# Performance work log

Hardware: AMD Instinct MI355X
Metric: run time of the kernel (lower is better)

## Reference

```python
import jax, jax.numpy as jnp
import numpy as np

NUDGE = 1e-7

def _norm(x):
    # global mean + L2-norm over axes (1,2), per sample (faithful to source)
    size = x.shape[1] * x.shape[2]
    mean = jnp.sum(x, axis=(1, 2), keepdims=True) / size
    xc = x - mean
    l2 = jnp.sqrt(jnp.sum(xc * xc, axis=(1, 2), keepdims=True))
    return xc / (l2 + NUDGE)


def setup_inputs() -> dict:
    key = jax.random.key(0)
    ks = jax.random.split(key, 9)
    B, D, S, F = 8, 512, 4096, 2048
    s = 0.02
    x = jax.random.normal(ks[0], (B, D, S), dtype=jnp.float32)
    Wq = jax.random.normal(ks[1], (D, D), dtype=jnp.float32) * s
    Wk = jax.random.normal(ks[2], (D, D), dtype=jnp.float32) * s
    Wv = jax.random.normal(ks[3], (D, D), dtype=jnp.float32) * s
    Wo = jax.random.normal(ks[4], (D, D), dtype=jnp.float32) * s
    W1 = jax.random.normal(ks[5], (D, F), dtype=jnp.float32) * s
    b1 = jnp.zeros((F,), dtype=jnp.float32)
    W2 = jax.random.normal(ks[6], (F, D), dtype=jnp.float32) * s
    b2 = jnp.zeros((D,), dtype=jnp.float32)
    return {"x": x, "Wq": Wq, "Wk": Wk, "Wv": Wv, "Wo": Wo,
            "W1": W1, "b1": b1, "W2": W2, "b2": b2}


def reference(x, Wq, Wk, Wv, Wo, W1, b1, W2, b2):
    B, D, S = x.shape
    xt = jnp.swapaxes(x, 1, 2)                      # [B,S,D]
    q = xt @ Wq                                     # [B,S,D]
    k = xt @ Wk
    v = xt @ Wv
    scores = jnp.einsum('bsd,btd->bst', q, k) / jnp.sqrt(jnp.float32(D))
    attn = jax.nn.softmax(scores, axis=-1)          # [B,S,S]
    attn_out = jnp.swapaxes((attn @ v) @ Wo, 1, 2)  # [B,D,S]

    post = _norm(x + attn_out)                      # [B,D,S]

    # per-slice feedforward+linear loop == batched matmul over token axis
    pt = jnp.swapaxes(post, 1, 2)                   # [B,S,D]
    h = jax.nn.relu(pt @ W1 + b1) @ W2 + b2         # [B,S,D]
    return _norm(post + jnp.swapaxes(h, 1, 2))
```

## Files before the change

### kernel.cpp

```cpp
#include <hip/hip_runtime.h>


typedef unsigned short u16;
typedef __attribute__((ext_vector_type(4))) float f32x4;
typedef __attribute__((ext_vector_type(8))) short s16x8;

__device__ __forceinline__ float bf2f(u16 u) {
    unsigned int v = ((unsigned int)u) << 16;
    float f;
    __builtin_memcpy(&f, &v, 4);
    return f;
}
__device__ __forceinline__ u16 f2bf(float f) {
    unsigned int v;
    __builtin_memcpy(&v, &f, 4);
    unsigned int r = (v + 0x7fffu + ((v >> 16) & 1u)) >> 16;
    return (u16)r;
}
__device__ __forceinline__ u16 loadbf(const void* p, long long i, int f32) {
    return f32 ? f2bf(((const float*)p)[i]) : ((const u16*)p)[i];
}

#if defined(__has_builtin)
#if __has_builtin(__builtin_amdgcn_global_load_lds)
#define HAS_GLDS 1
#endif
#endif
#ifndef HAS_GLDS
#define HAS_GLDS 0
#endif

#if HAS_GLDS
__device__ __forceinline__ void glds16(const u16* g, u16* l) {
    __builtin_amdgcn_global_load_lds(
        (const __attribute__((address_space(1))) void*)g,
        (__attribute__((address_space(3))) void*)l, 16, 0, 0);
}
#else
__device__ __forceinline__ void glds16(const u16* g, u16* l) {
    *(int4*)l = *(const int4*)g;
}
#endif

struct DetectArgs { const u16* p[9]; int n[9]; };

__global__ __launch_bounds__(256) void detect9(DetectArgs a, int* __restrict__ flags)
{
    const u16* p = a.p[blockIdx.x];
    const int n_u16 = a.n[blockIdx.x];
    int insane = 0;
    for (int i = threadIdx.x; i < n_u16; i += 256) {
        u16 h = p[i];
        int e = (h >> 7) & 0xFF;
        int m = h & 0x7F;
        bool sane = (e >= 96 && e <= 141) || (e == 0 && m == 0);
        insane += sane ? 0 : 1;
    }
#pragma unroll
    for (int off = 32; off > 0; off >>= 1) insane += __shfl_down(insane, off);
    __shared__ int red[4];
    if ((threadIdx.x & 63) == 0) red[threadIdx.x >> 6] = insane;
    __syncthreads();
    if (threadIdx.x == 0)
        flags[blockIdx.x] = (red[0] + red[1] + red[2] + red[3] > n_u16 / 4) ? 1 : 0;
}

#define BM 128
#define BN 128
#define BK 32

template <typename OutT, bool BIAS, bool RELU>
__global__ __launch_bounds__(256) void gemm_bt(
    const u16* __restrict__ A, const u16* __restrict__ Bt, OutT* __restrict__ C,
    const u16* __restrict__ bias, int M, int N, int K,
    int lda, int ldb, int ldc, int wmod,
    long long aZ, long long aW, long long bZ, long long bW, long long cZ,
    int swz)
{
    __shared__ u16 As[2][BM * BK];
    __shared__ u16 Bs[2][BN * BK];

    const int z = blockIdx.z;
    const int g = z / wmod, w = z - g * wmod;
    A  += g * aZ + w * aW;
    Bt += g * bZ + w * bW;
    C  += (long long)z * cZ;

    int bx = blockIdx.x, by = blockIdx.y;
    if (swz) {
        const int gx = gridDim.x;
        int id = by * gx + bx;
        int xcd = id & 7, j = id >> 3;
        bx = j % gx;
        by = (j / gx) * 8 + xcd;
    }

    const int tid = threadIdx.x;
    const int wave = tid >> 6, lane = tid & 63;
    const int wm = wave >> 1, wn = wave & 1;
    const int q = lane >> 4, r = lane & 15;

    const int ar = tid >> 2;
    const int ac = (((tid & 3) ^ ((tid >> 3) & 3)) << 3);
    const int ks = (r >> 1) & 3;

    const u16* Ag = A + (long long)(by * BM + ar) * lda + ac;
    const u16* Bg = Bt + (long long)(bx * BN + ar) * ldb + ac;
    const long long rstepA = 64LL * lda, rstepB = 64LL * ldb;

    f32x4 acc[4][4];
    const f32x4 zero = {0.f, 0.f, 0.f, 0.f};
#pragma unroll
    for (int i = 0; i < 4; ++i)
#pragma unroll
        for (int j = 0; j < 4; ++j) acc[i][j] = zero;

    const int nIter = K / BK;
    glds16(Ag, &As[0][tid * 8]);
    glds16(Ag + rstepA, &As[0][2048 + tid * 8]);
    glds16(Bg, &Bs[0][tid * 8]);
    glds16(Bg + rstepB, &Bs[0][2048 + tid * 8]);
    Ag += BK; Bg += BK;
    __syncthreads();
    for (int it = 0; it < nIter; ++it) {
        const int cur = it & 1, nxt = cur ^ 1;
        if (it + 1 < nIter) {
            glds16(Ag, &As[nxt][tid * 8]);
            glds16(Ag + rstepA, &As[nxt][2048 + tid * 8]);
            glds16(Bg, &Bs[nxt][tid * 8]);
            glds16(Bg + rstepB, &Bs[nxt][2048 + tid * 8]);
            Ag += BK; Bg += BK;
        }
        s16x8 af[4], bf[4];
#pragma unroll
        for (int mi = 0; mi < 4; ++mi)
            af[mi] = *(const s16x8*)(&As[cur][(wm * 64 + mi * 16 + r) * BK + ((q ^ ks) << 3)]);
#pragma unroll
        for (int ni = 0; ni < 4; ++ni)
            bf[ni] = *(const s16x8*)(&Bs[cur][(wn * 64 + ni * 16 + r) * BK + ((q ^ ks) << 3)]);
#pragma unroll
        for (int mi = 0; mi < 4; ++mi)
#pragma unroll
            for (int ni = 0; ni < 4; ++ni)
                acc[mi][ni] = __builtin_amdgcn_mfma_f32_16x16x32_bf16(
                    af[mi], bf[ni], acc[mi][ni], 0, 0, 0);
        __syncthreads();
    }

    const int col0 = bx * BN + wn * 64;
    const int row0 = by * BM + wm * 64;
#pragma unroll
    for (int ni = 0; ni < 4; ++ni) {
        const int colg = col0 + ni * 16 + r;
        float bv = 0.f;
        if constexpr (BIAS) bv = bf2f(bias[colg]);
#pragma unroll
        for (int mi = 0; mi < 4; ++mi) {
#pragma unroll
            for (int rr = 0; rr < 4; ++rr) {
                const int rowg = row0 + mi * 16 + q * 4 + rr;
                float v = acc[mi][ni][rr] + bv;
                if constexpr (RELU) v = fmaxf(v, 0.f);
                if constexpr (sizeof(OutT) == 2)
                    C[(long long)rowg * ldc + colg] = (OutT)f2bf(v);
                else
                    C[(long long)rowg * ldc + colg] = (OutT)v;
            }
        }
    }
}

template <bool DIRECT>
__global__ __attribute__((amdgpu_flat_work_group_size(512, 512)))
__attribute__((amdgpu_waves_per_eu(2, 2))) void flash_attn(
    const u16* __restrict__ QKV,
    const u16* __restrict__ Vt,
    u16* __restrict__ O,
    float* __restrict__ Opart,
    float* __restrict__ rsPart,
    int nsplit)
{
    __shared__ u16 Qs[64 * 256];
    __shared__ u16 Ks[2][128 * 128];
    __shared__ u16 Ps[64 * 136];
    __shared__ float rsL[8][64];

    const long long SD = 4096LL * 512;
    int g = blockIdx.z, qb = blockIdx.x;
    if (gridDim.z == 8 && gridDim.y == 1) {
        int id = g * 64 + qb;
        g = id & 7; qb = id >> 3;
    }
    const int sp = blockIdx.y;
    const int q0 = qb * 64;
    const u16* Qg = QKV + ((long long)g * 3 + 0) * SD;
    const u16* Kg = QKV + ((long long)g * 3 + 1) * SD;
    const u16* Vg = Vt + (long long)g * SD;

    const int tid = threadIdx.x;
    const int wave = tid >> 6, lane = tid & 63;
    const int q = lane >> 4, r = lane & 15;
    const int mg = wave >> 2, ng = wave & 3;
    const int dg = wave;

#pragma unroll
    for (int i = 0; i < 4; ++i) {
        int c = i * 512 + tid;
        int row = c >> 5, p = c & 31;
        int l = p ^ (row & 15);
        glds16(Qg + (long long)(q0 + row) * 512 + 256 + l * 8, &Qs[c * 8]);
    }

    const int span = 4096 / nsplit;
    const int kt0 = sp * span;
    const int ktN = span / 128;
    const float scale = 0.044194173824159216f;

    auto stageK = [&](int ktile, int kc, int buf) {
#pragma unroll
        for (int i = 0; i < 4; ++i) {
            int L = i * 512 + tid;
            int row = L >> 4, p = L & 15;
            int l = p ^ (row & 15);
            glds16(Kg + (long long)(kt0 + ktile * 128 + row) * 512 + kc * 128 + l * 8,
                   &Ks[buf][L * 8]);
        }
    };
    stageK(0, 0, 0);

    s16x8 qreg[2][8];
#pragma unroll
    for (int mi = 0; mi < 2; ++mi) {
        const long long row = q0 + (mg * 2 + mi) * 16 + r;
#pragma unroll
        for (int t = 0; t < 8; ++t)
            qreg[mi][t] = *(const s16x8*)(Qg + row * 512 + (t * 4 + q) * 8);
    }

    f32x4 oacc[4][4];
    const f32x4 zero = {0.f, 0.f, 0.f, 0.f};
#pragma unroll
    for (int i = 0; i < 4; ++i)
#pragma unroll
        for (int j = 0; j < 4; ++j) oacc[i][j] = zero;
    float rsum[2][4] = {{0.f, 0.f, 0.f, 0.f}, {0.f, 0.f, 0.f, 0.f}};

    for (int kt = 0; kt < ktN; ++kt) {
        f32x4 sacc[2][2];
#pragma unroll
        for (int i = 0; i < 2; ++i)
#pragma unroll
            for (int j = 0; j < 2; ++j) sacc[i][j] = zero;

#pragma unroll
        for (int kc = 0; kc < 2; ++kc) {
            __syncthreads();
            stageK(kt, kc + 1, (kc + 1) & 1);
            const u16* Kb = Ks[kc & 1];
#pragma unroll
            for (int sc = 0; sc < 4; ++sc) {
                s16x8 bf[2];
#pragma unroll
                for (int ni = 0; ni < 2; ++ni) {
                    int row = (ng * 2 + ni) * 16 + r;
                    int l = sc * 4 + q;
                    bf[ni] = *(const s16x8*)&Kb[row * 128 + ((l ^ r) << 3)];
                }
#pragma unroll
                for (int mi = 0; mi < 2; ++mi)
#pragma unroll
                    for (int ni = 0; ni < 2; ++ni)
                        sacc[mi][ni] = __builtin_amdgcn_mfma_f32_16x16x32_bf16(
                            qreg[mi][kc * 4 + sc], bf[ni], sacc[mi][ni], 0, 0, 0);
            }
        }
#pragma unroll
        for (int kc = 2; kc < 4; ++kc) {
            __syncthreads();
            if (kc < 3) stageK(kt, kc + 1, (kc + 1) & 1);
            const u16* Kb = Ks[kc & 1];
#pragma unroll
            for (int sc = 0; sc < 4; ++sc) {
                s16x8 af[2], bf[2];
#pragma unroll
                for (int mi = 0; mi < 2; ++mi) {
                    int row = (mg * 2 + mi) * 16 + r;
                    int l = (kc - 2) * 16 + sc * 4 + q;
                    af[mi] = *(const s16x8*)&Qs[row * 256 + ((l ^ r) << 3)];
                }
#pragma unroll
                for (int ni = 0; ni < 2; ++ni) {
                    int row = (ng * 2 + ni) * 16 + r;
                    int l = sc * 4 + q;
                    bf[ni] = *(const s16x8*)&Kb[row * 128 + ((l ^ r) << 3)];
                }
#pragma unroll
                for (int mi = 0; mi < 2; ++mi)
#pragma unroll
                    for (int ni = 0; ni < 2; ++ni)
                        sacc[mi][ni] = __builtin_amdgcn_mfma_f32_16x16x32_bf16(
                            af[mi], bf[ni], sacc[mi][ni], 0, 0, 0);
            }
        }
#pragma unroll
        for (int mi = 0; mi < 2; ++mi) {
#pragma unroll
            for (int ni = 0; ni < 2; ++ni) {
                int col = (ng * 2 + ni) * 16 + r;
#pragma unroll
                for (int rr = 0; rr < 4; ++rr) {
                    int row = (mg * 2 + mi) * 16 + q * 4 + rr;
                    float v = __expf(fminf(sacc[mi][ni][rr] * scale, 30.f));
                    Ps[row * 136 + col] = f2bf(v);
                    rsum[mi][rr] += v;
                }
            }
        }
        __syncthreads();
        if (kt + 1 < ktN) stageK(kt + 1, 0, 0);
        const long long vbase = (long long)(dg * 64 + r) * 4096 + kt0 + kt * 128;
#pragma unroll
        for (int kc = 0; kc < 4; ++kc) {
            s16x8 af[4], bf[4];
#pragma unroll
            for (int mi = 0; mi < 4; ++mi)
                af[mi] = *(const s16x8*)(Vg + vbase + (long long)mi * 16 * 4096
                                         + kc * 32 + q * 8);
#pragma unroll
            for (int ni = 0; ni < 4; ++ni)
                bf[ni] = *(const s16x8*)&Ps[(ni * 16 + r) * 136 + kc * 32 + q * 8];
            __builtin_amdgcn_s_setprio(1);
#pragma unroll
            for (int mi = 0; mi < 4; ++mi)
#pragma unroll
                for (int ni = 0; ni < 4; ++ni)
                    oacc[mi][ni] = __builtin_amdgcn_mfma_f32_16x16x32_bf16(
                        af[mi], bf[ni], oacc[mi][ni], 0, 0, 0);
            __builtin_amdgcn_s_setprio(0);
        }
    }

#pragma unroll
    for (int mi = 0; mi < 2; ++mi)
#pragma unroll
        for (int rr = 0; rr < 4; ++rr) {
            float s = rsum[mi][rr];
#pragma unroll
            for (int m = 1; m < 16; m <<= 1) s += __shfl_xor(s, m);
            rsum[mi][rr] = s;
        }
    if (r == 0) {
#pragma unroll
        for (int mi = 0; mi < 2; ++mi)
#pragma unroll
            for (int rr = 0; rr < 4; ++rr)
                rsL[wave][(mg * 2 + mi) * 16 + q * 4 + rr] = rsum[mi][rr];
    }
    __syncthreads();

    if constexpr (DIRECT) {
        u16* Og = O + (long long)g * SD;
#pragma unroll
        for (int ni = 0; ni < 4; ++ni) {
            int qrow = ni * 16 + r;
            int wb = (qrow >> 5) * 4;
            float rs = rsL[wb][qrow] + rsL[wb + 1][qrow]
                     + rsL[wb + 2][qrow] + rsL[wb + 3][qrow];
            float inv = 1.f / rs;
#pragma unroll
            for (int mi = 0; mi < 4; ++mi) {
                int d = (dg * 4 + mi) * 16 + q * 4;
                ushort4 o4;
                o4.x = f2bf(oacc[mi][ni][0] * inv);
                o4.y = f2bf(oacc[mi][ni][1] * inv);
                o4.z = f2bf(oacc[mi][ni][2] * inv);
                o4.w = f2bf(oacc[mi][ni][3] * inv);
                *(ushort4*)&Og[(long long)(q0 + qrow) * 512 + d] = o4;
            }
        }
    } else {
        const int pb = g * nsplit + sp;
        float* Op = Opart + (long long)pb * SD;
#pragma unroll
        for (int ni = 0; ni < 4; ++ni) {
            int qrow = ni * 16 + r;
#pragma unroll
            for (int mi = 0; mi < 4; ++mi) {
                int d = (dg * 4 + mi) * 16 + q * 4;
                float4 o4;
                o4.x = oacc[mi][ni][0]; o4.y = oacc[mi][ni][1];
                o4.z = oacc[mi][ni][2]; o4.w = oacc[mi][ni][3];
                *(float4*)&Op[(long long)(q0 + qrow) * 512 + d] = o4;
            }
        }
        if (tid < 64) {
            int wb = (tid >> 5) * 4;
            rsPart[(long long)pb * 4096 + q0 + tid] =
                rsL[wb][tid] + rsL[wb + 1][tid] + rsL[wb + 2][tid] + rsL[wb + 3][tid];
        }
    }
}

__global__ __launch_bounds__(256) void reduce_flash(
    const float* __restrict__ Opart, const float* __restrict__ rsPart,
    u16* __restrict__ O, int ns)
{
    const long long SD = 4096LL * 512;
    const int g = blockIdx.y;
    u16* Og = O + (long long)g * SD;
    const int base = blockIdx.x * 2048;
#pragma unroll
    for (int it = 0; it < 8; ++it) {
        int i = base + it * 256 + threadIdx.x;
        int row = i >> 9;
        float s = 0.f, rs = 0.f;
        for (int sp = 0; sp < ns; ++sp) {
            s += Opart[(long long)(g * ns + sp) * SD + i];
            rs += rsPart[(long long)(g * ns + sp) * 4096 + row];
        }
        Og[i] = f2bf(s / rs);
    }
}

__global__ __launch_bounds__(256) void transpose_any(
    const void* __restrict__ in, u16* __restrict__ out, int R, int C,
    long long sIn, long long sOut, const int* __restrict__ flag)
{
    __shared__ u16 tile[32][33];
    const int f32 = *flag;
    const long long ib = (long long)blockIdx.z * sIn;
    u16* ob = out + (long long)blockIdx.z * sOut;
    const int c0 = blockIdx.x * 32, r0 = blockIdx.y * 32;
    const int tx = threadIdx.x, ty = threadIdx.y;
#pragma unroll
    for (int i = 0; i < 4; ++i) {
        int rr = ty + i * 8;
        tile[rr][tx] = loadbf(in, ib + (long long)(r0 + rr) * C + c0 + tx, f32);
    }
    __syncthreads();
#pragma unroll
    for (int i = 0; i < 4; ++i) {
        int cc = ty + i * 8;
        ob[(long long)(c0 + cc) * R + r0 + tx] = tile[tx][cc];
    }
}

__global__ __launch_bounds__(256) void transpose_b16(
    const u16* __restrict__ in, u16* __restrict__ out, int R, int C,
    long long sIn, long long sOut)
{
    __shared__ u16 tile[32][33];
    in += (long long)blockIdx.z * sIn;
    out += (long long)blockIdx.z * sOut;
    const int c0 = blockIdx.x * 32, r0 = blockIdx.y * 32;
    const int tx = threadIdx.x, ty = threadIdx.y;
#pragma unroll
    for (int i = 0; i < 4; ++i) {
        int rr = ty + i * 8;
        tile[rr][tx] = in[(long long)(r0 + rr) * C + c0 + tx];
    }
    __syncthreads();
#pragma unroll
    for (int i = 0; i < 4; ++i) {
        int cc = ty + i * 8;
        out[(long long)(c0 + cc) * R + r0 + tx] = tile[tx][cc];
    }
}

__global__ __launch_bounds__(256) void convert_bias(
    const void* __restrict__ b1, const void* __restrict__ b2,
    u16* __restrict__ ob, const int* __restrict__ f1, const int* __restrict__ f2)
{
    int i = blockIdx.x * 256 + threadIdx.x;
    if (i < 2048) ob[i] = loadbf(b1, i, *f1);
    else if (i < 2560) ob[i] = loadbf(b2, i - 2048, *f2);
}

__global__ __launch_bounds__(256) void stats_add_partial(
    const u16* __restrict__ A, const u16* __restrict__ Bv,
    float2* __restrict__ partial)
{
    const int b = blockIdx.y;
    const long long yb = (long long)b * (4096LL * 512);
    const int base = blockIdx.x * 2048;
    float s = 0.f, ss = 0.f;
#pragma unroll
    for (int it = 0; it < 8; ++it) {
        int i = base + it * 256 + threadIdx.x;
        float z = bf2f(A[yb + i]) + bf2f(Bv[yb + i]);
        s += z; ss += z * z;
    }
#pragma unroll
    for (int off = 32; off > 0; off >>= 1) {
        s += __shfl_down(s, off); ss += __shfl_down(ss, off);
    }
    __shared__ float red[8];
    int lane = threadIdx.x & 63, wave = threadIdx.x >> 6;
    if (lane == 0) { red[wave * 2] = s; red[wave * 2 + 1] = ss; }
    __syncthreads();
    if (threadIdx.x == 0) {
        for (int w = 1; w < 4; ++w) { s += red[w * 2]; ss += red[w * 2 + 1]; }
        partial[b * 1024 + blockIdx.x] = make_float2(s, ss);
    }
}

__global__ __launch_bounds__(256) void stats_finish(
    const float2* __restrict__ partial, float2* __restrict__ stats, float N)
{
    const int b = blockIdx.x;
    float s = 0.f, ss = 0.f;
    for (int i = threadIdx.x; i < 1024; i += 256) {
        float2 p = partial[b * 1024 + i];
        s += p.x; ss += p.y;
    }
#pragma unroll
    for (int off = 32; off > 0; off >>= 1) {
        s += __shfl_down(s, off); ss += __shfl_down(ss, off);
    }
    __shared__ float red[8];
    int lane = threadIdx.x & 63, wave = threadIdx.x >> 6;
    if (lane == 0) { red[wave * 2] = s; red[wave * 2 + 1] = ss; }
    __syncthreads();
    if (threadIdx.x == 0) {
        for (int w = 1; w < 4; ++w) { s += red[w * 2]; ss += red[w * 2 + 1]; }
        float mean = s / N;
        float l2 = sqrtf(fmaxf(ss - s * s / N, 0.f));
        stats[b] = make_float2(mean, 1.f / (l2 + 1e-7f));
    }
}

__global__ __launch_bounds__(256) void post_kernel(
    const u16* __restrict__ A, const u16* __restrict__ Bv,
    const float2* __restrict__ stats, u16* __restrict__ post)
{
    const int b = blockIdx.y;
    const float2 st = stats[b];
    const long long yb = (long long)b * (4096LL * 512);
    const int base = blockIdx.x * 2048;
#pragma unroll
    for (int it = 0; it < 8; ++it) {
        int i = base + it * 256 + threadIdx.x;
        float z = bf2f(A[yb + i]) + bf2f(Bv[yb + i]);
        post[yb + i] = f2bf((z - st.x) * st.y);
    }
}

__global__ __launch_bounds__(256) void final_kernel(
    const u16* __restrict__ P, const u16* __restrict__ G,
    const float2* __restrict__ stats, float* __restrict__ out)
{
    __shared__ float tile[32][33];
    const int b = blockIdx.z;
    const float2 st = stats[b];
    const long long bb = (long long)b * (4096LL * 512);
    const int s0 = blockIdx.x * 32, d0 = blockIdx.y * 32;
    const int tx = threadIdx.x, ty = threadIdx.y;
#pragma unroll
    for (int i = 0; i < 4; ++i) {
        int sl = ty + i * 8;
        long long idx = bb + (long long)(s0 + sl) * 512 + d0 + tx;
        tile[sl][tx] = bf2f(P[idx]) + bf2f(G[idx]);
    }
    __syncthreads();
#pragma unroll
    for (int i = 0; i < 4; ++i) {
        int dl = ty + i * 8;
        out[bb + (long long)(d0 + dl) * 4096 + s0 + tx] =
            (tile[tx][dl] - st.x) * st.y;
    }
}

extern "C" void kernel_launch(void* const* d_in, const int* in_sizes, int n_in,
                              void* d_out, int out_size, void* d_ws, size_t ws_size,
                              hipStream_t stream)
{
    (void)out_size;
    const void* x  = d_in[0];
    const void* Wq = d_in[1];
    const void* Wk = d_in[2];
    const void* Wv = d_in[3];
    const void* Wo = d_in[4];
    const void* W1 = d_in[5];
    const void* b1 = d_in[6];
    const void* W2 = d_in[7];
    const void* b2 = d_in[8];

    const int Bb = 8, D = 512, S = 4096, F = 2048;
    const long long SD = (long long)S * D;
    const long long DD = (long long)D * D;

    char* ws = (char*)d_ws;
    size_t off = 0;
    auto take = [&](size_t bytes) -> char* {
        char* p = ws + off;
        off += (bytes + 255) & ~(size_t)255;
        return p;
    };
    u16* xt   = (u16*)take((size_t)Bb * SD * 2);
    u16* WqT  = (u16*)take((size_t)DD * 2);
    u16* WkT  = (u16*)take((size_t)DD * 2);
    u16* WvT  = (u16*)take((size_t)DD * 2);
    u16* WoT  = (u16*)take((size_t)DD * 2);
    u16* W1T  = (u16*)take((size_t)D * F * 2);
    u16* W2T  = (u16*)take((size_t)D * F * 2);
    u16* bb   = (u16*)take(2560 * 2);
    u16* post = (u16*)take((size_t)Bb * SD * 2);
    float2* npart  = (float2*)take(8 * 1024 * sizeof(float2));
    float2* stats1v = (float2*)take(256);
    float2* stats2v = (float2*)take(256);
    int* flags = (int*)take(16 * sizeof(int));
    float* rsPart = (float*)take(4 * 4096 * sizeof(float));

    size_t remaining = ws_size > off ? ws_size - off : 0;
    const size_t perG = (size_t)4 * SD * 2 + 4096;
    int G = (remaining >= 8 * perG) ? 8 : (remaining >= 4 * perG) ? 4 : 2;
    int ns = (G >= 4) ? 1 : 2;

    u16* attnBuf = (u16*)take((size_t)4 * G * SD * 2);
    u16* QKVb = attnBuf;
    u16* Vtb  = attnBuf + (size_t)3 * G * SD;
    float* Opart = (float*)post;
    u16* Oall = (u16*)d_out;
    u16* Y    = post;
    u16* Hbuf = (u16*)d_out;
    u16* Gbuf = attnBuf;

    DetectArgs da;
    for (int i = 0; i < 9; ++i) {
        da.p[i] = (const u16*)d_in[i];
        da.n[i] = (i < n_in && in_sizes[i] < 8192) ? in_sizes[i] : 8192;
    }
    detect9<<<dim3(9), 256, 0, stream>>>(da, flags);

    dim3 tb(32, 8, 1);
    transpose_any<<<dim3(S / 32, D / 32, Bb), tb, 0, stream>>>(x, xt, D, S, SD, SD, flags + 0);
    transpose_any<<<dim3(16, 16, 1), tb, 0, stream>>>(Wq, WqT, D, D, 0, 0, flags + 1);
    transpose_any<<<dim3(16, 16, 1), tb, 0, stream>>>(Wk, WkT, D, D, 0, 0, flags + 2);
    transpose_any<<<dim3(16, 16, 1), tb, 0, stream>>>(Wv, WvT, D, D, 0, 0, flags + 3);
    transpose_any<<<dim3(16, 16, 1), tb, 0, stream>>>(Wo, WoT, D, D, 0, 0, flags + 4);
    transpose_any<<<dim3(F / 32, D / 32, 1), tb, 0, stream>>>(W1, W1T, D, F, 0, 0, flags + 5);
    transpose_any<<<dim3(D / 32, F / 32, 1), tb, 0, stream>>>(W2, W2T, F, D, 0, 0, flags + 7);
    convert_bias<<<10, 256, 0, stream>>>(b1, b2, bb, flags + 6, flags + 8);

    for (int b0 = 0; b0 < Bb; b0 += G) {
        gemm_bt<u16, false, false><<<dim3(D / 128, S / 128, 3 * G), 256, 0, stream>>>(
            xt + (long long)b0 * SD, WqT, QKVb, nullptr, S, D, D, D, D, D,
            3, SD, 0, 0, DD, SD, 1);
        transpose_b16<<<dim3(D / 32, S / 32, G), tb, 0, stream>>>(
            QKVb + 2 * SD, Vtb, S, D, 3 * SD, SD);
        if (ns == 1) {
            flash_attn<true><<<dim3(64, 1, G), 512, 0, stream>>>(
                QKVb, Vtb, Oall + (long long)b0 * SD, nullptr, nullptr, 1);
        } else {
            flash_attn<false><<<dim3(64, ns, G), 512, 0, stream>>>(
                QKVb, Vtb, nullptr, Opart, rsPart, ns);
            reduce_flash<<<dim3(1024, G), 256, 0, stream>>>(
                Opart, rsPart, Oall + (long long)b0 * SD, ns);
        }
    }

    gemm_bt<u16, false, false><<<dim3(D / 128, (Bb * S) / 128, 1), 256, 0, stream>>>(
        Oall, WoT, Y, nullptr, Bb * S, D, D, D, D, D, 1, 0, 0, 0, 0, 0, 1);

    stats_add_partial<<<dim3(1024, Bb), 256, 0, stream>>>(xt, Y, npart);
    stats_finish<<<dim3(Bb), 256, 0, stream>>>(npart, stats1v, (float)SD);
    post_kernel<<<dim3(1024, Bb), 256, 0, stream>>>(xt, Y, stats1v, post);

    for (int h = 0; h < 2; ++h) {
        gemm_bt<u16, true, true><<<dim3(F / 128, (4 * S) / 128, 1), 256, 0, stream>>>(
            post + (long long)h * 4 * SD, W1T, Hbuf, bb, 4 * S, F, D, D, D, F,
            1, 0, 0, 0, 0, 0, 1);
        gemm_bt<u16, true, false><<<dim3(D / 128, (4 * S) / 128, 1), 256, 0, stream>>>(
            Hbuf, W2T, Gbuf + (long long)h * 4 * SD, bb + 2048, 4 * S, D, F, F, F, D,
            1, 0, 0, 0, 0, 0, 1);
    }

    stats_add_partial<<<dim3(1024, Bb), 256, 0, stream>>>(post, Gbuf, npart);
    stats_finish<<<dim3(Bb), 256, 0, stream>>>(npart, stats2v, (float)SD);
    final_kernel<<<dim3(S / 32, D / 32, Bb), tb, 0, stream>>>(
        post, Gbuf, stats2v, (float*)d_out);
}
```

Before: 1.033 ms.

## Triple-buffer K tiles in flash attention with vmcnt-gated barriers

The flash attention kernel now stages K chunks into a three-slot LDS ring with a prefetch depth of two, and this continues across key-tile boundaries instead of restarting after the P·V phase. Plain __syncthreads are replaced by barriers that wait only until four global loads remain outstanding (s_waitcnt vmcnt(4)), or only on LDS counters. The intent is to hide K load latency behind the QK^T MFMAs and the P·V phase. The cost is about 32KB more LDS. Prefetches past the last tile read beyond the split's key range, and the scheme depends on exact in-flight load counts for correctness.

```diff
diff --git a/kernel.cpp b/kernel.cpp
--- a/kernel.cpp
+++ b/kernel.cpp
@@ -41,6 +41,19 @@
     *(int4*)l = *(const int4*)g;
 }
 #endif
+
+__device__ __forceinline__ void bar_vmcnt4() {
+    asm volatile("s_waitcnt vmcnt(4)" ::: "memory");
+    __builtin_amdgcn_sched_barrier(0);
+    __builtin_amdgcn_s_barrier();
+    __builtin_amdgcn_sched_barrier(0);
+}
+__device__ __forceinline__ void bar_lds() {
+    asm volatile("s_waitcnt lgkmcnt(0)" ::: "memory");
+    __builtin_amdgcn_sched_barrier(0);
+    __builtin_amdgcn_s_barrier();
+    __builtin_amdgcn_sched_barrier(0);
+}
 
 struct DetectArgs { const u16* p[9]; int n[9]; };
 
@@ -171,8 +184,7 @@
 }
 
 template <bool DIRECT>
-__global__ __attribute__((amdgpu_flat_work_group_size(512, 512)))
-__attribute__((amdgpu_waves_per_eu(2, 2))) void flash_attn(
+__global__ __launch_bounds__(512, 2) void flash_attn(
     const u16* __restrict__ QKV,
     const u16* __restrict__ Vt,
     u16* __restrict__ O,
@@ -181,7 +193,7 @@
     int nsplit)
 {
     __shared__ u16 Qs[64 * 256];
-    __shared__ u16 Ks[2][128 * 128];
+    __shared__ u16 Ks[3][128 * 128];
     __shared__ u16 Ps[64 * 136];
     __shared__ float rsL[8][64];
 
@@ -203,6 +215,20 @@
     const int mg = wave >> 2, ng = wave & 3;
     const int dg = wave;
 
+    const int span = 4096 / nsplit;
+    const int kt0 = sp * span;
+    const int ktN = span / 128;
+    const float scale = 0.044194173824159216f;
+
+    s16x8 qreg[2][8];
+#pragma unroll
+    for (int mi = 0; mi < 2; ++mi) {
+        const long long row = q0 + (mg * 2 + mi) * 16 + r;
+#pragma unroll
+        for (int t = 0; t < 8; ++t)
+            qreg[mi][t] = *(const s16x8*)(Qg + row * 512 + (t * 4 + q) * 8);
+    }
+
 #pragma unroll
     for (int i = 0; i < 4; ++i) {
         int c = i * 512 + tid;
@@ -211,31 +237,18 @@
         glds16(Qg + (long long)(q0 + row) * 512 + 256 + l * 8, &Qs[c * 8]);
     }
 
-    const int span = 4096 / nsplit;
-    const int kt0 = sp * span;
-    const int ktN = span / 128;
-    const float scale = 0.044194173824159216f;
-
-    auto stageK = [&](int ktile, int kc, int buf) {
+    auto stageK = [&](int c) {
 #pragma unroll
         for (int i = 0; i < 4; ++i) {
             int L = i * 512 + tid;
             int row = L >> 4, p = L & 15;
             int l = p ^ (row & 15);
-            glds16(Kg + (long long)(kt0 + ktile * 128 + row) * 512 + kc * 128 + l * 8,
-                   &Ks[buf][L * 8]);
+            glds16(Kg + (long long)(kt0 + (c >> 2) * 128 + row) * 512 + (c & 3) * 128 + l * 8,
+                   &Ks[c % 3][L * 8]);
         }
     };
-    stageK(0, 0, 0);
-
-    s16x8 qreg[2][8];
-#pragma unroll
-    for (int mi = 0; mi < 2; ++mi) {
-        const long long row = q0 + (mg * 2 + mi) * 16 + r;
-#pragma unroll
-        for (int t = 0; t < 8; ++t)
-            qreg[mi][t] = *(const s16x8*)(Qg + row * 512 + (t * 4 + q) * 8);
-    }
+    stageK(0);
+    stageK(1);
 
     f32x4 oacc[4][4];
     const f32x4 zero = {0.f, 0.f, 0.f, 0.f};
@@ -254,9 +267,9 @@
 
 #pragma unroll
         for (int kc = 0; kc < 2; ++kc) {
-            __syncthreads();
-            stageK(kt, kc + 1, (kc + 1) & 1);
-            const u16* Kb = Ks[kc & 1];
+            bar_vmcnt4();
+            stageK(kt * 4 + kc + 2);
+            const u16* Kb = Ks[(kt * 4 + kc) % 3];
 #pragma unroll
             for (int sc = 0; sc < 4; ++sc) {
                 s16x8 bf[2];
@@ -276,9 +289,9 @@
         }
 #pragma unroll
         for (int kc = 2; kc < 4; ++kc) {
-            __syncthreads();
-            if (kc < 3) stageK(kt, kc + 1, (kc + 1) & 1);
-            const u16* Kb = Ks[kc & 1];
+            bar_vmcnt4();
+            stageK(kt * 4 + kc + 2);
+            const u16* Kb = Ks[(kt * 4 + kc) % 3];
 #pragma unroll
             for (int sc = 0; sc < 4; ++sc) {
                 s16x8 af[2], bf[2];
@@ -316,8 +329,7 @@
                 }
             }
         }
-        __syncthreads();
-        if (kt + 1 < ktN) stageK(kt + 1, 0, 0);
+        bar_lds();
         const long long vbase = (long long)(dg * 64 + r) * 4096 + kt0 + kt * 128;
 #pragma unroll
         for (int kc = 0; kc < 4; ++kc) {
```

Measured after the change: 1.073 ms. 1.04x slower.
